# Performance work log

Hardware: AMD Instinct MI355X
Metric: run time of the kernel (lower is better)

Reference implementation:

```python
import jax, jax.numpy as jnp
import numpy as np

BATCH = 2048
DIM = 1024       # discrete_dim
EMBED = 512
HID = 2 * EMBED  # MLP hidden width per source: [embed_dim*2, embed_dim*2, discrete_dim]
NUM_STEPS = 32


def setup_inputs() -> dict:
    key = jax.random.key(0)
    ks = jax.random.split(key, 8)
    s = 0.02  # init scale for weights
    init_samples = jax.random.randint(ks[0], (BATCH, DIM), 0, 2).astype(jnp.float32)
    target_pos = jax.random.randint(ks[1], (NUM_STEPS, BATCH), 0, DIM, dtype=jnp.int32)
    W1 = jax.random.normal(ks[2], (DIM, HID), jnp.float32) * s
    b1 = jnp.zeros((HID,), jnp.float32)
    W2 = jax.random.normal(ks[3], (HID, HID), jnp.float32) * s
    b2 = jnp.zeros((HID,), jnp.float32)
    W3 = jax.random.normal(ks[4], (HID, DIM), jnp.float32) * s
    b3 = jnp.zeros((DIM,), jnp.float32)
    return {
        "init_samples": init_samples, "target_pos": target_pos,
        "W1": W1, "b1": b1, "W2": W2, "b2": b2, "W3": W3, "b3": b3,
        "num_steps": NUM_STEPS,
    }


def _mlp(x, W1, b1, W2, b2, W3, b3):
    h = jax.nn.relu(x @ W1 + b1)
    h = jax.nn.relu(h @ W2 + b2)
    return h @ W3 + b3  # pos logits, [B, DIM]


def reference(init_samples, target_pos, W1, b1, W2, b2, W3, b3, num_steps):
    B = init_samples.shape[0]
    rows = jnp.arange(B)
    very_init_samples = init_samples
    total_log0 = jnp.zeros((B, 1), init_samples.dtype)  # mode != 'forward': total_log = 0.0

    def step(carry, tpos):
        samples, total_log = carry
        log_pos_prob = jax.nn.log_softmax(_mlp(samples, W1, b1, W2, b2, W3, b3), axis=-1)
        log_target = jnp.take_along_axis(log_pos_prob, tpos[:, None], axis=1)  # [B,1]
        total_log = total_log + log_target
        orig_bit = samples[rows, tpos]                       # gather, [B]
        samples = samples.at[rows, tpos].set(1.0 - orig_bit)  # scatter bit flip
        return (samples, total_log), tpos

    (final_samples, total_log), delta = jax.lax.scan(
        step, (init_samples, total_log0), target_pos[:num_steps])
    return final_samples, delta, total_log, very_init_samples
```

## Files before the change

kernel.cpp:

```cpp
#include <hip/hip_runtime.h>
#include <stdint.h>

#define BATCH 2048
#define NDIM  1024
#define HID   1024
#define TSTEPS 32

#define OUT_FINAL 0
#define OUT_DELTA 2097152
#define OUT_TOTAL 2162688
#define OUT_VINIT 2164736

#define SC_ROWSUM 0
#define SC_TGT    8192
#define SC_TOTAL  16384
#define SC_BIAS   24576
#define SC_FLAG   36864

#define WF_WT1    0u
#define WF_WT2    2097152u
#define WF_WT3    4194304u
#define WF_A1     6291456u
#define WF_BIAS   14680064u
#define WF_SIGNS  14692352u
#define WF_ROWSUM 14757888u
#define WF_TGT    15020032u
#define WF_FLAG   15282176u
#define WF_H1     15286272u

__device__ __forceinline__ float bf2f(ushort u) {
  union { uint32_t u; float f; } v; v.u = ((uint32_t)u) << 16; return v.f;
}
__device__ __forceinline__ ushort f2bf(float f) {
  union { float f; uint32_t u; } v; v.f = f;
  uint32_t u = v.u;
  u += 0x7fffu + ((u >> 16) & 1u);
  return (ushort)(u >> 16);
}

typedef __attribute__((ext_vector_type(8))) short bf16x8;
typedef __attribute__((ext_vector_type(8))) unsigned short u16x8;
typedef __attribute__((ext_vector_type(4))) float f32x4;

__device__ __forceinline__ void gload_lds16(const void* g, void* l) {
  __builtin_amdgcn_global_load_lds((const __attribute__((address_space(1))) void*)g,
                                   (__attribute__((address_space(3))) void*)l, 16, 0, 0);
}

__global__ __launch_bounds__(256) void flag_k(const void* __restrict__ init,
                                              uint32_t* __restrict__ flag) {
  const ushort* p = (const ushort*)init;
  __shared__ uint32_t acc[256];
  uint32_t a = 0;
  for (int i = threadIdx.x; i < 32768; i += 256) a |= p[2 * i];
  acc[threadIdx.x] = a;
  __syncthreads();
  for (int s = 128; s > 0; s >>= 1) {
    if (threadIdx.x < s) acc[threadIdx.x] |= acc[threadIdx.x + s];
    __syncthreads();
  }
  if (threadIdx.x == 0) *flag = (acc[0] != 0) ? 1u : 0u;
}

__global__ __launch_bounds__(256) void zero_k(float* __restrict__ p) {
  p[blockIdx.x * 256 + threadIdx.x] = 0.f;
}

__global__ __launch_bounds__(256) void canon_b_k(const void* b1, const void* b2,
                                                 const void* b3,
                                                 float* __restrict__ dst,
                                                 const uint32_t* __restrict__ flag) {
  const void* src = (blockIdx.x == 0) ? b1 : (blockIdx.x == 1) ? b2 : b3;
  float* d = dst + blockIdx.x * 1024;
  const bool isbf = (*flag != 0);
  for (int i = threadIdx.x; i < 1024; i += 256)
    d[i] = isbf ? bf2f(((const ushort*)src)[i]) : ((const float*)src)[i];
}

__global__ __launch_bounds__(256) void canon_w3_k(const void* __restrict__ S1,
                                                  const void* __restrict__ S2,
                                                  const void* __restrict__ S3,
                                                  ushort* __restrict__ D,
                                                  const uint32_t* __restrict__ flag) {
  __shared__ ushort tile[32][33];
  const void* S = (blockIdx.z == 0) ? S1 : (blockIdx.z == 1) ? S2 : S3;
  ushort* Dz = D + (size_t)blockIdx.z * 1024 * 1024;
  const int bx = blockIdx.x * 32, by = blockIdx.y * 32;
  const int tx = threadIdx.x, ty = threadIdx.y;
  const bool isbf = (*flag != 0);
  #pragma unroll
  for (int i = 0; i < 32; i += 8) {
    const size_t idx = (size_t)(by + ty + i) * 1024 + bx + tx;
    tile[ty + i][tx] = isbf ? ((const ushort*)S)[idx] : f2bf(((const float*)S)[idx]);
  }
  __syncthreads();
  #pragma unroll
  for (int i = 0; i < 32; i += 8)
    Dz[(size_t)(bx + ty + i) * 1024 + by + tx] = tile[tx][ty + i];
}

__global__ __launch_bounds__(256) void sign_k(const void* __restrict__ init,
                                              const int* __restrict__ tpos,
                                              uint8_t* __restrict__ signs,
                                              float* __restrict__ rowsum,
                                              float* __restrict__ tgt,
                                              const uint32_t* __restrict__ flag) {
  const int m = blockIdx.x, tid = threadIdx.x;
  const bool isbf = (*flag != 0);
  __shared__ float bits[NDIM];
  #pragma unroll
  for (int i = 0; i < 4; ++i) {
    const int k = tid + i * 256;
    bits[k] = isbf ? bf2f(((const ushort*)init)[(size_t)m * NDIM + k])
                   : ((const float*)init)[(size_t)m * NDIM + k];
  }
  __syncthreads();
  if (tid == 0) {
    for (int t = 0; t < TSTEPS; ++t) {
      const int tp = tpos[t * BATCH + m];
      const float b = bits[tp];
      signs[t * BATCH + m] = (uint8_t)(b != 0.f);
      bits[tp] = 1.f - b;
    }
  }
  if (tid < 32) rowsum[m * 32 + tid] = 0.f;
  else if (tid < 64) tgt[m * 32 + (tid - 32)] = 0.f;
}

template <int ASTAGE, int EPI>
__global__ __launch_bounds__(512) void gemm_bt(const void* __restrict__ A,
                                               const ushort* __restrict__ Bt,
                                               const float* __restrict__ bias,
                                               void* __restrict__ Cout,
                                               const int* __restrict__ tpos,
                                               float* __restrict__ rowsum,
                                               float* __restrict__ tgt,
                                               const uint32_t* __restrict__ flag,
                                               int rowbase) {
  constexpr int BM = 128, BN = 128, BK = 32, K = 1024;
  __shared__ ushort Asm[BM * BK];
  __shared__ ushort Bsm[BN * BK];
  const int tid = threadIdx.x;
  const int w = tid >> 6, lane = tid & 63;
  const int q = lane >> 4, r = lane & 15;

  const int lid = blockIdx.y * gridDim.x + blockIdx.x;
  const int xcd = lid & 7;
  const int sl  = lid >> 3;
  const int mb  = xcd + 8 * (sl >> 3);
  const int nb  = sl & 7;
  const int n0 = nb * BN;
  const int m0 = mb * BM;
  const int wm = (w & 1) * 64;
  const int wn = (w >> 1) * 32;

  f32x4 acc[4][2];
  #pragma unroll
  for (int i = 0; i < 4; ++i)
    #pragma unroll
    for (int j = 0; j < 2; ++j)
      #pragma unroll
      for (int e = 0; e < 4; ++e) acc[i][j][e] = 0.f;

  const int row = tid >> 2, c8 = (tid & 3) * 8;
  const bool isbf = (ASTAGE == 1) ? (*flag != 0) : true;

  for (int k0 = 0; k0 < K; k0 += BK) {
    if constexpr (ASTAGE == 0) {
      gload_lds16((const char*)A + ((size_t)(m0 + row) * K + k0 + c8) * 2,
                  (char*)Asm + tid * 16);
    } else {
      u16x8 av;
      if (isbf) {
        av = *(const u16x8*)((const ushort*)A + (size_t)(m0 + row) * K + k0 + c8);
      } else {
        const float* fp = (const float*)A + (size_t)(m0 + row) * K + k0 + c8;
        const float4 fa = *(const float4*)fp, fb = *(const float4*)(fp + 4);
        av[0] = f2bf(fa.x); av[1] = f2bf(fa.y); av[2] = f2bf(fa.z); av[3] = f2bf(fa.w);
        av[4] = f2bf(fb.x); av[5] = f2bf(fb.y); av[6] = f2bf(fb.z); av[7] = f2bf(fb.w);
      }
      *(u16x8*)((char*)Asm + tid * 16) = av;
    }
    gload_lds16((const char*)Bt + ((size_t)(n0 + row) * K + k0 + c8) * 2,
                (char*)Bsm + tid * 16);
    __syncthreads();
    bf16x8 af[4], bfr[2];
    #pragma unroll
    for (int t = 0; t < 4; ++t)
      af[t] = *(const bf16x8*)(Asm + (wm + t * 16 + r) * BK + q * 8);
    #pragma unroll
    for (int t = 0; t < 2; ++t)
      bfr[t] = *(const bf16x8*)(Bsm + (wn + t * 16 + r) * BK + q * 8);
    #pragma unroll
    for (int mt = 0; mt < 4; ++mt)
      #pragma unroll
      for (int nt = 0; nt < 2; ++nt)
        acc[mt][nt] = __builtin_amdgcn_mfma_f32_16x16x32_bf16(af[mt], bfr[nt], acc[mt][nt], 0, 0, 0);
    __syncthreads();
  }

  #pragma unroll
  for (int mt = 0; mt < 4; ++mt) {
    #pragma unroll
    for (int reg = 0; reg < 4; ++reg) {
      const int grow = m0 + wm + mt * 16 + q * 4 + reg;
      if constexpr (EPI == 2) {
        const int growg = rowbase + grow;
        const int tp = tpos[growg];
        float s2 = 0.f;
        #pragma unroll
        for (int nt = 0; nt < 2; ++nt) {
          const int gcol = n0 + wn + nt * 16 + r;
          const float v = acc[mt][nt][reg] + bias[gcol];
          if (gcol == tp) tgt[growg] = v;
          s2 += __expf(v);
        }
        s2 += __shfl_xor(s2, 1);
        s2 += __shfl_xor(s2, 2);
        s2 += __shfl_xor(s2, 4);
        s2 += __shfl_xor(s2, 8);
        if (r == 0) atomicAdd(&rowsum[growg], s2);
      } else {
        #pragma unroll
        for (int nt = 0; nt < 2; ++nt) {
          const int gcol = n0 + wn + nt * 16 + r;
          const float v = acc[mt][nt][reg] + bias[gcol];
          if constexpr (EPI == 0) {
            ((float*)Cout)[(size_t)grow * NDIM + gcol] = v;
          } else {
            ((ushort*)Cout)[(size_t)grow * NDIM + gcol] = f2bf(v > 0.f ? v : 0.f);
          }
        }
      }
    }
  }
}

__global__ __launch_bounds__(256) void build_h1(float* __restrict__ a1,
                                                const void* __restrict__ W1,
                                                const uint8_t* __restrict__ signs,
                                                const int* __restrict__ tpos,
                                                ushort* __restrict__ h1,
                                                const uint32_t* __restrict__ flag,
                                                int t0, int nsteps) {
  const int m = blockIdx.x;
  const int k = threadIdx.x * 4;
  const bool isbf = (*flag != 0);
  float4 a = *(const float4*)(a1 + (size_t)m * HID + k);
  for (int t = 0; t < nsteps; ++t) {
    ushort4 h;
    h.x = f2bf(a.x > 0.f ? a.x : 0.f);
    h.y = f2bf(a.y > 0.f ? a.y : 0.f);
    h.z = f2bf(a.z > 0.f ? a.z : 0.f);
    h.w = f2bf(a.w > 0.f ? a.w : 0.f);
    *(ushort4*)(h1 + ((size_t)(t * BATCH + m)) * HID + k) = h;
    const int tg = t0 + t;
    const int tp = tpos[tg * BATCH + m];
    const float s = 1.f - 2.f * (float)signs[tg * BATCH + m];
    float wx, wy, wz, ww;
    if (isbf) {
      const ushort4 wv = *(const ushort4*)((const ushort*)W1 + (size_t)tp * HID + k);
      wx = bf2f(wv.x); wy = bf2f(wv.y); wz = bf2f(wv.z); ww = bf2f(wv.w);
    } else {
      const float4 wv = *(const float4*)((const float*)W1 + (size_t)tp * HID + k);
      wx = wv.x; wy = wv.y; wz = wv.z; ww = wv.w;
    }
    a.x += s * wx; a.y += s * wy; a.z += s * wz; a.w += s * ww;
  }
  *(float4*)(a1 + (size_t)m * HID + k) = a;
}

__global__ __launch_bounds__(256) void outputs_k(const void* __restrict__ init,
                                                 const int* __restrict__ tpos,
                                                 const float* __restrict__ tgt,
                                                 const float* __restrict__ rowsum,
                                                 float* __restrict__ out,
                                                 const uint32_t* __restrict__ flag) {
  const int m = blockIdx.x;
  const int tid = threadIdx.x;
  const int k = tid * 4;
  const bool isbf = (*flag != 0);
  float v[4];
  if (isbf) {
    const ushort4 iv = *(const ushort4*)((const ushort*)init + (size_t)m * NDIM + k);
    v[0] = bf2f(iv.x); v[1] = bf2f(iv.y); v[2] = bf2f(iv.z); v[3] = bf2f(iv.w);
  } else {
    const float4 iv = *(const float4*)((const float*)init + (size_t)m * NDIM + k);
    v[0] = iv.x; v[1] = iv.y; v[2] = iv.z; v[3] = iv.w;
  }
  float4 o0; o0.x = v[0]; o0.y = v[1]; o0.z = v[2]; o0.w = v[3];
  *(float4*)(out + OUT_VINIT + (size_t)m * NDIM + k) = o0;
  for (int t = 0; t < TSTEPS; ++t) {
    const int tp = tpos[t * BATCH + m];
    if ((tp >> 2) == tid) v[tp & 3] = 1.f - v[tp & 3];
  }
  float4 o; o.x = v[0]; o.y = v[1]; o.z = v[2]; o.w = v[3];
  *(float4*)(out + OUT_FINAL + (size_t)m * NDIM + k) = o;
  if (tid < 32) out[OUT_DELTA + m * 32 + tid] = (float)tpos[m * 32 + tid];
  if (tid < 64) {
    const int t = tid & 31;
    float s = tgt[t * BATCH + m] - logf(rowsum[t * BATCH + m]);
    s += __shfl_xor(s, 1, 32);
    s += __shfl_xor(s, 2, 32);
    s += __shfl_xor(s, 4, 32);
    s += __shfl_xor(s, 8, 32);
    s += __shfl_xor(s, 16, 32);
    if (tid == 0) out[OUT_TOTAL + m] = s;
  }
}

template <int ASRC, int EPI>
__global__ __launch_bounds__(256) void gemm_t(const void* __restrict__ A,
                                              const void* __restrict__ W,
                                              const float* __restrict__ bias,
                                              ushort* __restrict__ Cout,
                                              const int* __restrict__ tpos,
                                              float* __restrict__ rowsum,
                                              float* __restrict__ tgt,
                                              const uint32_t* __restrict__ flag,
                                              int tstep) {
  constexpr int BM = 64, BN = 64, BK = 32, BKP = 40, K = 1024;
  __shared__ ushort Asm[BM * BKP];
  __shared__ ushort Bsm[BN * BKP];
  const int tid = threadIdx.x;
  const int w = tid >> 6, lane = tid & 63;
  const int q = lane >> 4, r = lane & 15;
  const int n0 = blockIdx.x * BN;
  const int m0 = blockIdx.y * BM;
  const bool isbf = (*flag != 0);
  const int srow = tid >> 2, scol = (tid & 3) * 8;
  const int kk = tid >> 3, ng = (tid & 7) * 8;

  f32x4 acc[4];
  #pragma unroll
  for (int nt = 0; nt < 4; ++nt)
    #pragma unroll
    for (int e = 0; e < 4; ++e) acc[nt][e] = 0.f;

  for (int k0 = 0; k0 < K; k0 += BK) {
    u16x8 av;
    if constexpr (ASRC == 0) {
      if (isbf) {
        av = *(const u16x8*)((const ushort*)A + (size_t)(m0 + srow) * K + k0 + scol);
      } else {
        const float* fp = (const float*)A + (size_t)(m0 + srow) * K + k0 + scol;
        const float4 fa = *(const float4*)fp, fb = *(const float4*)(fp + 4);
        av[0] = f2bf(fa.x); av[1] = f2bf(fa.y); av[2] = f2bf(fa.z); av[3] = f2bf(fa.w);
        av[4] = f2bf(fb.x); av[5] = f2bf(fb.y); av[6] = f2bf(fb.z); av[7] = f2bf(fb.w);
      }
    } else {
      av = *(const u16x8*)((const ushort*)A + (size_t)(m0 + srow) * K + k0 + scol);
      if constexpr (ASRC == 1) {
        #pragma unroll
        for (int e = 0; e < 8; ++e) av[e] = (av[e] & 0x8000u) ? (unsigned short)0 : av[e];
      }
    }
    ushort bw[8];
    if (isbf) {
      const u16x8 wv = *(const u16x8*)((const ushort*)W + (size_t)(k0 + kk) * NDIM + n0 + ng);
      #pragma unroll
      for (int j = 0; j < 8; ++j) bw[j] = wv[j];
    } else {
      const float* fp = (const float*)W + (size_t)(k0 + kk) * NDIM + n0 + ng;
      const float4 fa = *(const float4*)fp, fb = *(const float4*)(fp + 4);
      bw[0] = f2bf(fa.x); bw[1] = f2bf(fa.y); bw[2] = f2bf(fa.z); bw[3] = f2bf(fa.w);
      bw[4] = f2bf(fb.x); bw[5] = f2bf(fb.y); bw[6] = f2bf(fb.z); bw[7] = f2bf(fb.w);
    }
    __syncthreads();
    *(u16x8*)(Asm + srow * BKP + scol) = av;
    #pragma unroll
    for (int j = 0; j < 8; ++j) Bsm[(ng + j) * BKP + kk] = bw[j];
    __syncthreads();
    const bf16x8 af = *(const bf16x8*)(Asm + (w * 16 + r) * BKP + q * 8);
    #pragma unroll
    for (int nt = 0; nt < 4; ++nt) {
      const bf16x8 bfr = *(const bf16x8*)(Bsm + (nt * 16 + r) * BKP + q * 8);
      acc[nt] = __builtin_amdgcn_mfma_f32_16x16x32_bf16(af, bfr, acc[nt], 0, 0, 0);
    }
  }

  if constexpr (EPI == 2) {
    #pragma unroll
    for (int reg = 0; reg < 4; ++reg) {
      const int grow = m0 + w * 16 + q * 4 + reg;
      const int tp = tpos[tstep * BATCH + grow];
      float s = 0.f;
      #pragma unroll
      for (int nt = 0; nt < 4; ++nt) {
        const int gcol = n0 + nt * 16 + r;
        const float v = acc[nt][reg] + bias[gcol];
        if (gcol == tp) tgt[grow] = v;
        s += __expf(v);
      }
      s += __shfl_xor(s, 1);
      s += __shfl_xor(s, 2);
      s += __shfl_xor(s, 4);
      s += __shfl_xor(s, 8);
      if (r == 0) atomicAdd(&rowsum[grow], s);
    }
  } else {
    #pragma unroll
    for (int nt = 0; nt < 4; ++nt) {
      #pragma unroll
      for (int reg = 0; reg < 4; ++reg) {
        const int grow = m0 + w * 16 + q * 4 + reg;
        const int gcol = n0 + nt * 16 + r;
        float v = acc[nt][reg] + bias[gcol];
        if constexpr (EPI == 1) v = (v > 0.f) ? v : 0.f;
        Cout[(size_t)grow * NDIM + gcol] = f2bf(v);
      }
    }
  }
}

__global__ __launch_bounds__(256) void step_k(ushort* __restrict__ a1,
                                              const void* __restrict__ init,
                                              const void* __restrict__ W1,
                                              const int* __restrict__ tpos,
                                              float* __restrict__ rowsum,
                                              const float* __restrict__ tgt,
                                              float* __restrict__ total,
                                              const uint32_t* __restrict__ flag,
                                              int t) {
  const int m = blockIdx.x;
  const int k = threadIdx.x * 4;
  const bool isbf = (*flag != 0);
  const int tp = tpos[t * BATCH + m];
  const float b0 = isbf ? bf2f(((const ushort*)init)[(size_t)m * NDIM + tp])
                        : ((const float*)init)[(size_t)m * NDIM + tp];
  int cnt = 0;
  for (int u = 0; u < t; ++u) cnt += (tpos[u * BATCH + m] == tp) ? 1 : 0;
  const float bit = (cnt & 1) ? (1.f - b0) : b0;
  const float s = 1.f - 2.f * bit;
  float wx, wy, wz, ww;
  if (isbf) {
    const ushort4 wv = *(const ushort4*)((const ushort*)W1 + (size_t)tp * HID + k);
    wx = bf2f(wv.x); wy = bf2f(wv.y); wz = bf2f(wv.z); ww = bf2f(wv.w);
  } else {
    const float4 wv = *(const float4*)((const float*)W1 + (size_t)tp * HID + k);
    wx = wv.x; wy = wv.y; wz = wv.z; ww = wv.w;
  }
  ushort4 a = *(const ushort4*)(a1 + (size_t)m * HID + k);
  a.x = f2bf(bf2f(a.x) + s * wx);
  a.y = f2bf(bf2f(a.y) + s * wy);
  a.z = f2bf(bf2f(a.z) + s * wz);
  a.w = f2bf(bf2f(a.w) + s * ww);
  *(ushort4*)(a1 + (size_t)m * HID + k) = a;
  if (threadIdx.x == 0) {
    total[m] += tgt[m] - logf(rowsum[m]);
    rowsum[m] = 0.f;
  }
}

__global__ __launch_bounds__(256) void finalize_k(const float* __restrict__ total,
                                                  float* __restrict__ out_total) {
  const int m = blockIdx.x * 256 + threadIdx.x;
  out_total[m] = total[m];
}

__global__ __launch_bounds__(256) void out_final_k(const void* __restrict__ init,
                                                   const int* __restrict__ tpos,
                                                   float* __restrict__ out,
                                                   const uint32_t* __restrict__ flag) {
  const int m = blockIdx.x;
  const int k = threadIdx.x * 4;
  const bool isbf = (*flag != 0);
  float v[4];
  if (isbf) {
    const ushort4 iv = *(const ushort4*)((const ushort*)init + (size_t)m * NDIM + k);
    v[0] = bf2f(iv.x); v[1] = bf2f(iv.y); v[2] = bf2f(iv.z); v[3] = bf2f(iv.w);
  } else {
    const float4 iv = *(const float4*)((const float*)init + (size_t)m * NDIM + k);
    v[0] = iv.x; v[1] = iv.y; v[2] = iv.z; v[3] = iv.w;
  }
  for (int t = 0; t < TSTEPS; ++t) {
    const int tp = tpos[t * BATCH + m];
    if ((tp >> 2) == (int)threadIdx.x) v[tp & 3] = 1.f - v[tp & 3];
  }
  float4 o; o.x = v[0]; o.y = v[1]; o.z = v[2]; o.w = v[3];
  *(float4*)(out + OUT_FINAL + (size_t)m * NDIM + k) = o;
}

__global__ __launch_bounds__(256) void out_vinit_k(const void* __restrict__ init,
                                                   float* __restrict__ out,
                                                   const uint32_t* __restrict__ flag) {
  const int i = (blockIdx.x * 256 + threadIdx.x) * 4;
  float4 o;
  if (*flag) {
    const ushort4 iv = *(const ushort4*)((const ushort*)init + i);
    o.x = bf2f(iv.x); o.y = bf2f(iv.y); o.z = bf2f(iv.z); o.w = bf2f(iv.w);
  } else {
    o = *(const float4*)((const float*)init + i);
  }
  *(float4*)(out + OUT_VINIT + i) = o;
}

__global__ __launch_bounds__(256) void out_delta_k(const int* __restrict__ tpos,
                                                   float* __restrict__ out) {
  const int i = blockIdx.x * 256 + threadIdx.x;
  out[OUT_DELTA + i] = (float)tpos[i];
}

extern "C" void kernel_launch(void* const* d_in, const int* in_sizes, int n_in,
                              void* d_out, int out_size, void* d_ws, size_t ws_size,
                              hipStream_t stream) {
  const void* init = d_in[0];
  const int* tpos  = (const int*)d_in[1];
  const void* W1 = d_in[2];
  const void* b1 = d_in[3];
  const void* W2 = d_in[4];
  const void* b2 = d_in[5];
  const void* W3 = d_in[6];
  const void* b3 = d_in[7];
  float* out = (float*)d_out;
  char* ws = (char*)d_ws;

  const size_t MB = 1024ull * 1024ull;
  int CH = TSTEPS;
  while (CH > 1 && (size_t)WF_H1 + (size_t)CH * 8 * MB > ws_size) CH >>= 1;
  const bool fast = (ws_size >= (size_t)WF_H1 + 8 * MB);

  if (fast) {
    ushort*   WT1    = (ushort*)(ws + WF_WT1);
    ushort*   WT2    = (ushort*)(ws + WF_WT2);
    ushort*   WT3    = (ushort*)(ws + WF_WT3);
    float*    a1f    = (float*)(ws + WF_A1);
    float*    biases = (float*)(ws + WF_BIAS);
    uint8_t*  signs  = (uint8_t*)(ws + WF_SIGNS);
    float*    rowsum = (float*)(ws + WF_ROWSUM);
    float*    tgt    = (float*)(ws + WF_TGT);
    uint32_t* flag   = (uint32_t*)(ws + WF_FLAG);
    ushort*   h1     = (ushort*)(ws + WF_H1);
    ushort*   h2     = (ushort*)(ws + WF_H1 + (size_t)CH * 4 * MB);

    flag_k<<<1, 256, 0, stream>>>(init, flag);
    canon_b_k<<<3, 256, 0, stream>>>(b1, b2, b3, biases, flag);
    canon_w3_k<<<dim3(32, 32, 3), dim3(32, 8), 0, stream>>>(W1, W2, W3, WT1, flag);
    sign_k<<<BATCH, 256, 0, stream>>>(init, tpos, signs, rowsum, tgt, flag);

    gemm_bt<1, 0><<<dim3(8, 16), 512, 0, stream>>>(init, WT1, biases + 0, a1f,
                                                   nullptr, nullptr, nullptr, flag, 0);

    for (int t0 = 0; t0 < TSTEPS; t0 += CH) {
      build_h1<<<BATCH, 256, 0, stream>>>(a1f, W1, signs, tpos, h1, flag, t0, CH);
      gemm_bt<0, 1><<<dim3(8, CH * 16), 512, 0, stream>>>(h1, WT2, biases + 1024, h2,
                                                          nullptr, nullptr, nullptr, flag, 0);
      gemm_bt<0, 2><<<dim3(8, CH * 16), 512, 0, stream>>>(h2, WT3, biases + 2048, nullptr,
                                                          tpos, rowsum, tgt, flag, t0 * BATCH);
    }
    outputs_k<<<BATCH, 256, 0, stream>>>(init, tpos, tgt, rowsum, out, flag);
  } else {
    ushort*   a1     = (ushort*)(out + OUT_FINAL);
    ushort*   h2     = (ushort*)(out + OUT_VINIT);
    char*     sc     = (char*)(out + OUT_DELTA);
    float*    rowsum = (float*)(sc + SC_ROWSUM);
    float*    tgt    = (float*)(sc + SC_TGT);
    float*    total  = (float*)(sc + SC_TOTAL);
    float*    biases = (float*)(sc + SC_BIAS);
    uint32_t* flag   = (uint32_t*)(sc + SC_FLAG);

    flag_k<<<1, 256, 0, stream>>>(init, flag);
    zero_k<<<24, 256, 0, stream>>>(rowsum);
    canon_b_k<<<3, 256, 0, stream>>>(b1, b2, b3, biases, flag);
    gemm_t<0, 0><<<dim3(16, 32), 256, 0, stream>>>(init, W1, biases + 0, a1,
                                                   nullptr, nullptr, nullptr, flag, 0);
    for (int t = 0; t < TSTEPS; ++t) {
      gemm_t<1, 1><<<dim3(16, 32), 256, 0, stream>>>(a1, W2, biases + 1024, h2,
                                                     nullptr, nullptr, nullptr, flag, 0);
      gemm_t<2, 2><<<dim3(16, 32), 256, 0, stream>>>(h2, W3, biases + 2048, nullptr,
                                                     tpos, rowsum, tgt, flag, t);
      step_k<<<BATCH, 256, 0, stream>>>(a1, init, W1, tpos, rowsum, tgt, total, flag, t);
    }
    finalize_k<<<8, 256, 0, stream>>>(total, out + OUT_TOTAL);
    out_final_k<<<BATCH, 256, 0, stream>>>(init, tpos, out, flag);
    out_vinit_k<<<2048, 256, 0, stream>>>(init, out, flag);
    out_delta_k<<<256, 256, 0, stream>>>(tpos, out);
  }
}
```

Baseline: 573.5 us.

## Run hidden-layer GEMMs in FP8 with quantized weights and activations

Quantizes the second and third layer weights to FP8 during the transpose pass. Hidden activations are stored as FP8 instead of bf16. A new 128x128-tile GEMM kernel then uses the fp8 MFMA instruction for those two layers. This roughly halves the memory traffic for the activation buffers and raises matrix throughput. In exchange, FP8 rounding lowers the precision of the logits.

```diff
diff --git a/kernel.cpp b/kernel.cpp
--- a/kernel.cpp
+++ b/kernel.cpp
@@ -18,15 +18,15 @@
 #define SC_FLAG   36864
 
 #define WF_WT1    0u
-#define WF_WT2    2097152u
-#define WF_WT3    4194304u
-#define WF_A1     6291456u
-#define WF_BIAS   14680064u
-#define WF_SIGNS  14692352u
-#define WF_ROWSUM 14757888u
-#define WF_TGT    15020032u
-#define WF_FLAG   15282176u
-#define WF_H1     15286272u
+#define WF_W2Q    2097152u
+#define WF_W3Q    3145728u
+#define WF_A1     4194304u
+#define WF_BIAS   12582912u
+#define WF_SIGNS  12595200u
+#define WF_ROWSUM 12660736u
+#define WF_TGT    12922880u
+#define WF_FLAG   13185024u
+#define WF_H1     13189120u
 
 __device__ __forceinline__ float bf2f(ushort u) {
   union { uint32_t u; float f; } v; v.u = ((uint32_t)u) << 16; return v.f;
@@ -36,6 +36,12 @@
   uint32_t u = v.u;
   u += 0x7fffu + ((u >> 16) & 1u);
   return (ushort)(u >> 16);
+}
+__device__ __forceinline__ uint32_t f2fp8x2(float a, float b) {
+  return (uint32_t)__builtin_amdgcn_cvt_pk_fp8_f32(a, b, 0, false) & 0xffffu;
+}
+__device__ __forceinline__ uint8_t f2fp8(float a) {
+  return (uint8_t)(__builtin_amdgcn_cvt_pk_fp8_f32(a, a, 0, false) & 0xff);
 }
 
 typedef __attribute__((ext_vector_type(8))) short bf16x8;
@@ -80,23 +86,35 @@
 __global__ __launch_bounds__(256) void canon_w3_k(const void* __restrict__ S1,
                                                   const void* __restrict__ S2,
                                                   const void* __restrict__ S3,
-                                                  ushort* __restrict__ D,
+                                                  ushort* __restrict__ WT1,
+                                                  uint8_t* __restrict__ WQ,
                                                   const uint32_t* __restrict__ flag) {
-  __shared__ ushort tile[32][33];
-  const void* S = (blockIdx.z == 0) ? S1 : (blockIdx.z == 1) ? S2 : S3;
-  ushort* Dz = D + (size_t)blockIdx.z * 1024 * 1024;
+  __shared__ float tile[32][33];
+  const int z = blockIdx.z;
+  const void* S = (z == 0) ? S1 : (z == 1) ? S2 : S3;
   const int bx = blockIdx.x * 32, by = blockIdx.y * 32;
   const int tx = threadIdx.x, ty = threadIdx.y;
   const bool isbf = (*flag != 0);
   #pragma unroll
   for (int i = 0; i < 32; i += 8) {
     const size_t idx = (size_t)(by + ty + i) * 1024 + bx + tx;
-    tile[ty + i][tx] = isbf ? ((const ushort*)S)[idx] : f2bf(((const float*)S)[idx]);
+    tile[ty + i][tx] = isbf ? bf2f(((const ushort*)S)[idx]) : ((const float*)S)[idx];
   }
   __syncthreads();
-  #pragma unroll
-  for (int i = 0; i < 32; i += 8)
-    Dz[(size_t)(bx + ty + i) * 1024 + by + tx] = tile[tx][ty + i];
+  if (z == 0) {
+    #pragma unroll
+    for (int i = 0; i < 32; i += 8)
+      WT1[(size_t)(bx + ty + i) * 1024 + by + tx] = f2bf(tile[tx][ty + i]);
+  } else {
+    uint8_t* Dz = WQ + (size_t)(z - 1) * 1024 * 1024;
+    #pragma unroll
+    for (int i = 0; i < 32; i += 8) {
+      if (tx < 16) {
+        const float lo = tile[2 * tx][ty + i], hi = tile[2 * tx + 1][ty + i];
+        *(ushort*)(Dz + (size_t)(bx + ty + i) * 1024 + by + 2 * tx) = (ushort)f2fp8x2(lo, hi);
+      }
+    }
+  }
 }
 
 __global__ __launch_bounds__(256) void sign_k(const void* __restrict__ init,
@@ -204,12 +222,91 @@
     #pragma unroll
     for (int reg = 0; reg < 4; ++reg) {
       const int grow = m0 + wm + mt * 16 + q * 4 + reg;
+      #pragma unroll
+      for (int nt = 0; nt < 2; ++nt) {
+        const int gcol = n0 + wn + nt * 16 + r;
+        const float v = acc[mt][nt][reg] + bias[gcol];
+        if constexpr (EPI == 0) {
+          ((float*)Cout)[(size_t)grow * NDIM + gcol] = v;
+        } else {
+          ((ushort*)Cout)[(size_t)grow * NDIM + gcol] = f2bf(v > 0.f ? v : 0.f);
+        }
+      }
+    }
+  }
+}
+
+template <int EPI>
+__global__ __launch_bounds__(256) void gemm_fp8(const uint8_t* __restrict__ A,
+                                                const uint8_t* __restrict__ Bt,
+                                                const float* __restrict__ bias,
+                                                uint8_t* __restrict__ Cout,
+                                                const int* __restrict__ tpos,
+                                                float* __restrict__ rowsum,
+                                                float* __restrict__ tgt,
+                                                int rowbase) {
+  constexpr int BM = 128, BN = 128, BK = 64, K = 1024;
+  __shared__ uint8_t Asm[BM * BK];
+  __shared__ uint8_t Bsm[BN * BK];
+  const int tid = threadIdx.x;
+  const int wave = tid >> 6, lane = tid & 63;
+  const int q = lane >> 4, r = lane & 15;
+
+  const int lid = blockIdx.y * gridDim.x + blockIdx.x;
+  const int xcd = lid & 7;
+  const int sl  = lid >> 3;
+  const int mb  = xcd + 8 * (sl >> 3);
+  const int nb  = sl & 7;
+  const int n0 = nb * BN;
+  const int m0 = mb * BM;
+  const int wm = (wave & 1) * 64, wn = (wave >> 1) * 64;
+
+  f32x4 acc[4][4];
+  #pragma unroll
+  for (int i = 0; i < 4; ++i)
+    #pragma unroll
+    for (int j = 0; j < 4; ++j)
+      #pragma unroll
+      for (int e = 0; e < 4; ++e) acc[i][j][e] = 0.f;
+
+  const int f0 = tid * 16, f1 = f0 + 4096;
+  const int row0 = f0 >> 6, kb0 = f0 & 63;
+  const int row1 = f1 >> 6, kb1 = f1 & 63;
+
+  for (int k0 = 0; k0 < K; k0 += BK) {
+    gload_lds16(A + (size_t)(m0 + row0) * K + k0 + kb0, Asm + f0);
+    gload_lds16(A + (size_t)(m0 + row1) * K + k0 + kb1, Asm + f1);
+    gload_lds16(Bt + (size_t)(n0 + row0) * K + k0 + kb0, Bsm + f0);
+    gload_lds16(Bt + (size_t)(n0 + row1) * K + k0 + kb1, Bsm + f1);
+    __syncthreads();
+    #pragma unroll
+    for (int s = 0; s < 2; ++s) {
+      long af[4], bfr[4];
+      #pragma unroll
+      for (int t = 0; t < 4; ++t) {
+        af[t]  = *(const long*)(Asm + (wm + t * 16 + r) * BK + s * 32 + q * 8);
+        bfr[t] = *(const long*)(Bsm + (wn + t * 16 + r) * BK + s * 32 + q * 8);
+      }
+      #pragma unroll
+      for (int mt = 0; mt < 4; ++mt)
+        #pragma unroll
+        for (int nt = 0; nt < 4; ++nt)
+          acc[mt][nt] = __builtin_amdgcn_mfma_f32_16x16x32_fp8_fp8(af[mt], bfr[nt], acc[mt][nt], 0, 0, 0);
+    }
+    __syncthreads();
+  }
+
+  #pragma unroll
+  for (int mt = 0; mt < 4; ++mt) {
+    #pragma unroll
+    for (int reg = 0; reg < 4; ++reg) {
+      const int grow = m0 + wm + mt * 16 + q * 4 + reg;
       if constexpr (EPI == 2) {
         const int growg = rowbase + grow;
         const int tp = tpos[growg];
         float s2 = 0.f;
         #pragma unroll
-        for (int nt = 0; nt < 2; ++nt) {
+        for (int nt = 0; nt < 4; ++nt) {
           const int gcol = n0 + wn + nt * 16 + r;
           const float v = acc[mt][nt][reg] + bias[gcol];
           if (gcol == tp) tgt[growg] = v;
@@ -222,14 +319,10 @@
         if (r == 0) atomicAdd(&rowsum[growg], s2);
       } else {
         #pragma unroll
-        for (int nt = 0; nt < 2; ++nt) {
+        for (int nt = 0; nt < 4; ++nt) {
           const int gcol = n0 + wn + nt * 16 + r;
           const float v = acc[mt][nt][reg] + bias[gcol];
-          if constexpr (EPI == 0) {
-            ((float*)Cout)[(size_t)grow * NDIM + gcol] = v;
-          } else {
-            ((ushort*)Cout)[(size_t)grow * NDIM + gcol] = f2bf(v > 0.f ? v : 0.f);
-          }
+          Cout[(size_t)grow * NDIM + gcol] = f2fp8(v > 0.f ? v : 0.f);
         }
       }
     }
@@ -240,7 +333,7 @@
                                                 const void* __restrict__ W1,
                                                 const uint8_t* __restrict__ signs,
                                                 const int* __restrict__ tpos,
-                                                ushort* __restrict__ h1,
+                                                uint8_t* __restrict__ h1,
                                                 const uint32_t* __restrict__ flag,
                                                 int t0, int nsteps) {
   const int m = blockIdx.x;
@@ -248,12 +341,12 @@
   const bool isbf = (*flag != 0);
   float4 a = *(const float4*)(a1 + (size_t)m * HID + k);
   for (int t = 0; t < nsteps; ++t) {
-    ushort4 h;
-    h.x = f2bf(a.x > 0.f ? a.x : 0.f);
-    h.y = f2bf(a.y > 0.f ? a.y : 0.f);
-    h.z = f2bf(a.z > 0.f ? a.z : 0.f);
-    h.w = f2bf(a.w > 0.f ? a.w : 0.f);
-    *(ushort4*)(h1 + ((size_t)(t * BATCH + m)) * HID + k) = h;
+    const float r0 = a.x > 0.f ? a.x : 0.f;
+    const float r1 = a.y > 0.f ? a.y : 0.f;
+    const float r2 = a.z > 0.f ? a.z : 0.f;
+    const float r3 = a.w > 0.f ? a.w : 0.f;
+    const uint32_t word = f2fp8x2(r0, r1) | (f2fp8x2(r2, r3) << 16);
+    *(uint32_t*)(h1 + (size_t)(t * BATCH + m) * HID + k) = word;
     const int tg = t0 + t;
     const int tp = tpos[tg * BATCH + m];
     const float s = 1.f - 2.f * (float)signs[tg * BATCH + m];
@@ -517,25 +610,26 @@
 
   const size_t MB = 1024ull * 1024ull;
   int CH = TSTEPS;
-  while (CH > 1 && (size_t)WF_H1 + (size_t)CH * 8 * MB > ws_size) CH >>= 1;
-  const bool fast = (ws_size >= (size_t)WF_H1 + 8 * MB);
+  while (CH > 1 && (size_t)WF_H1 + (size_t)CH * 4 * MB > ws_size) CH >>= 1;
+  const bool fast = (ws_size >= (size_t)WF_H1 + 4 * MB);
 
   if (fast) {
     ushort*   WT1    = (ushort*)(ws + WF_WT1);
-    ushort*   WT2    = (ushort*)(ws + WF_WT2);
-    ushort*   WT3    = (ushort*)(ws + WF_WT3);
+    uint8_t*  WQ     = (uint8_t*)(ws + WF_W2Q);
+    uint8_t*  W2Q    = (uint8_t*)(ws + WF_W2Q);
+    uint8_t*  W3Q    = (uint8_t*)(ws + WF_W3Q);
     float*    a1f    = (float*)(ws + WF_A1);
     float*    biases = (float*)(ws + WF_BIAS);
     uint8_t*  signs  = (uint8_t*)(ws + WF_SIGNS);
     float*    rowsum = (float*)(ws + WF_ROWSUM);
     float*    tgt    = (float*)(ws + WF_TGT);
     uint32_t* flag   = (uint32_t*)(ws + WF_FLAG);
-    ushort*   h1     = (ushort*)(ws + WF_H1);
-    ushort*   h2     = (ushort*)(ws + WF_H1 + (size_t)CH * 4 * MB);
+    uint8_t*  h1     = (uint8_t*)(ws + WF_H1);
+    uint8_t*  h2     = (uint8_t*)(ws + WF_H1 + (size_t)CH * 2 * MB);
 
     flag_k<<<1, 256, 0, stream>>>(init, flag);
     canon_b_k<<<3, 256, 0, stream>>>(b1, b2, b3, biases, flag);
-    canon_w3_k<<<dim3(32, 32, 3), dim3(32, 8), 0, stream>>>(W1, W2, W3, WT1, flag);
+    canon_w3_k<<<dim3(32, 32, 3), dim3(32, 8), 0, stream>>>(W1, W2, W3, WT1, WQ, flag);
     sign_k<<<BATCH, 256, 0, stream>>>(init, tpos, signs, rowsum, tgt, flag);
 
     gemm_bt<1, 0><<<dim3(8, 16), 512, 0, stream>>>(init, WT1, biases + 0, a1f,
@@ -543,10 +637,10 @@
 
     for (int t0 = 0; t0 < TSTEPS; t0 += CH) {
       build_h1<<<BATCH, 256, 0, stream>>>(a1f, W1, signs, tpos, h1, flag, t0, CH);
-      gemm_bt<0, 1><<<dim3(8, CH * 16), 512, 0, stream>>>(h1, WT2, biases + 1024, h2,
-                                                          nullptr, nullptr, nullptr, flag, 0);
-      gemm_bt<0, 2><<<dim3(8, CH * 16), 512, 0, stream>>>(h2, WT3, biases + 2048, nullptr,
-                                                          tpos, rowsum, tgt, flag, t0 * BATCH);
+      gemm_fp8<1><<<dim3(8, CH * 16), 256, 0, stream>>>(h1, W2Q, biases + 1024, h2,
+                                                        nullptr, nullptr, nullptr, 0);
+      gemm_fp8<2><<<dim3(8, CH * 16), 256, 0, stream>>>(h2, W3Q, biases + 2048, nullptr,
+                                                        tpos, rowsum, tgt, t0 * BATCH);
     }
     outputs_k<<<BATCH, 256, 0, stream>>>(init, tpos, tgt, rowsum, out, flag);
   } else {
```

Result: slower. 820.8 us (+43.1%).
